# Optimization experiments

Hardware: AMD Instinct MI355X
Metric: run time of the kernel (lower is better)

The kernel has to match this reference:

```python
import jax, jax.numpy as jnp
import numpy as np
import math

N_HEAD = 16
N_EMBED = 1024
BLOCK_SIZE = 2048


def setup_inputs() -> dict:
    key = jax.random.key(0)
    k0, k1, k2, k3, k4 = jax.random.split(key, 5)
    B, T, C = 2, 2048, N_EMBED
    x = jax.random.normal(k0, (B, T, C), dtype=jnp.float32)
    # torch nn.Linear weights: [out_features, in_features]
    s_attn = 1.0 / math.sqrt(C)
    W_attn = jax.random.uniform(k1, (3 * C, C), dtype=jnp.float32, minval=-s_attn, maxval=s_attn)
    b_attn = jax.random.uniform(k2, (3 * C,), dtype=jnp.float32, minval=-s_attn, maxval=s_attn)
    W_proj = jax.random.uniform(k3, (C, C), dtype=jnp.float32, minval=-s_attn, maxval=s_attn)
    b_proj = jax.random.uniform(k4, (C,), dtype=jnp.float32, minval=-s_attn, maxval=s_attn)
    return {"x": x, "W_attn": W_attn, "b_attn": b_attn, "W_proj": W_proj, "b_proj": b_proj}


def reference(x, W_attn, b_attn, W_proj, b_proj):
    B, T, C = x.shape
    H = N_HEAD
    D = C // H
    qkv = x @ W_attn.T + b_attn                     # [B,T,3C]
    q, k, v = jnp.split(qkv, 3, axis=2)
    # [B,T,C] -> [B,H,T,D]
    q = q.reshape(B, T, H, D).transpose(0, 2, 1, 3)
    k = k.reshape(B, T, H, D).transpose(0, 2, 1, 3)
    v = v.reshape(B, T, H, D).transpose(0, 2, 1, 3)
    scale = 1.0 / math.sqrt(D)
    attn = jnp.einsum('bhqd,bhkd->bhqk', q, k) * scale   # [B,H,T,T]
    causal = jnp.tril(jnp.ones((T, T), dtype=bool))
    attn = jnp.where(causal[None, None, :, :], attn, -jnp.inf)
    attn = jax.nn.softmax(attn, axis=-1)
    y = jnp.einsum('bhqk,bhkd->bhqd', attn, v)           # [B,H,T,D]
    y = y.transpose(0, 2, 1, 3).reshape(B, T, C)
    return y @ W_proj.T + b_proj
```

## Files before the change

### kernel.cpp

```cpp
#include <hip/hip_runtime.h>
#include <hip/hip_bf16.h>

#define B_  2
#define T_  2048
#define C_  1024
#define H_  16
#define D_  64
#define M_  (B_*T_)
#define N1_ (3*C_)

typedef short bf16x8 __attribute__((ext_vector_type(8)));
typedef short bf16x4 __attribute__((ext_vector_type(4)));
typedef float f32x4 __attribute__((ext_vector_type(4)));
typedef unsigned short u16;
typedef u16 u16x8 __attribute__((ext_vector_type(8)));

#define QSCALE 0.18033688011112042f
#define C8     11.541560327111707f

__device__ __forceinline__ u16 f2bf(float f) {
  unsigned u = __float_as_uint(f);
  u += 0x7FFFu + ((u >> 16) & 1u);
  return (u16)(u >> 16);
}

__device__ __forceinline__ void gload16(const void* g, void* l) {
  __builtin_amdgcn_global_load_lds((__attribute__((address_space(1))) void*)g,
                                   (__attribute__((address_space(3))) void*)l,
                                   16, 0, 0);
}

__global__ __launch_bounds__(256) void cvt3(const float* __restrict__ x,
                                            const float* __restrict__ wa,
                                            const float* __restrict__ wp,
                                            u16* __restrict__ out) {
  int i = (blockIdx.x * 256 + threadIdx.x) * 8;
  const float* src;
  int off;
  if (i < M_ * C_)                 { src = x;  off = 0; }
  else if (i < M_ * C_ + N1_ * C_) { src = wa; off = M_ * C_; }
  else                             { src = wp; off = M_ * C_ + N1_ * C_; }
  float4 a = *(const float4*)(src + (i - off));
  float4 b = *(const float4*)(src + (i - off) + 4);
  u16x8 o;
  o[0] = f2bf(a.x); o[1] = f2bf(a.y); o[2] = f2bf(a.z); o[3] = f2bf(a.w);
  o[4] = f2bf(b.x); o[5] = f2bf(b.y); o[6] = f2bf(b.z); o[7] = f2bf(b.w);
  *(u16x8*)(out + i) = o;
}

__device__ __forceinline__ void gemm_core(const u16* __restrict__ A,
                                          const u16* __restrict__ W,
                                          u16* As, u16* Bs,
                                          f32x4 (&acc)[4][4],
                                          int m0, int n0, int K) {
  int tid = threadIdx.x;
  int lane = tid & 63, wid = tid >> 6;
  int wr = wid >> 1, wc = wid & 1;

  int arow = wid * 16 + (lane >> 2);
  int ag = lane & 3;
  int sg = ag ^ ((arow >> 1) & 3);
  const u16* aSrc0 = A + (m0 + arow) * K + sg * 8;
  const u16* aSrc1 = aSrc0 + 64 * K;
  const u16* bSrc0 = W + (n0 + arow) * K + sg * 8;
  const u16* bSrc1 = bSrc0 + 64 * K;
  u16* aDst0 = As + (wid * 16) * 32;
  u16* aDst1 = As + (64 + wid * 16) * 32;
  u16* bDst0 = Bs + (wid * 16) * 32;
  u16* bDst1 = Bs + (64 + wid * 16) * 32;

  int rg = lane >> 4;
  int aoff[4], boff[4];
#pragma unroll
  for (int m = 0; m < 4; ++m) {
    int row = wr * 64 + m * 16 + (lane & 15);
    aoff[m] = row * 32 + (rg ^ ((row >> 1) & 3)) * 8;
    row = wc * 64 + m * 16 + (lane & 15);
    boff[m] = row * 32 + (rg ^ ((row >> 1) & 3)) * 8;
  }

  for (int kt = 0; kt < K / 32; ++kt) {
    int k0 = kt * 32;
    __syncthreads();
    gload16(aSrc0 + k0, aDst0);
    gload16(aSrc1 + k0, aDst1);
    gload16(bSrc0 + k0, bDst0);
    gload16(bSrc1 + k0, bDst1);
    __syncthreads();

    bf16x8 af[4], bfr[4];
#pragma unroll
    for (int m = 0; m < 4; ++m) af[m] = *(const bf16x8*)(As + aoff[m]);
#pragma unroll
    for (int n = 0; n < 4; ++n) bfr[n] = *(const bf16x8*)(Bs + boff[n]);
#pragma unroll
    for (int m = 0; m < 4; ++m)
#pragma unroll
      for (int n = 0; n < 4; ++n)
        acc[m][n] = __builtin_amdgcn_mfma_f32_16x16x32_bf16(af[m], bfr[n], acc[m][n], 0, 0, 0);
  }
}

__global__ __launch_bounds__(256) void gemm_qkv(const u16* __restrict__ A,
                                                const u16* __restrict__ W,
                                                const float* __restrict__ bias,
                                                u16* __restrict__ Qb,
                                                u16* __restrict__ Kb,
                                                u16* __restrict__ Vt) {
  __shared__ __align__(16) u16 As[128 * 32];
  __shared__ __align__(16) u16 Bs[128 * 32];
  f32x4 acc[4][4] = {};
  int m0 = blockIdx.x * 128, n0 = blockIdx.y * 128;
  gemm_core(A, W, As, Bs, acc, m0, n0, C_);

  int lane = threadIdx.x & 63, wid = threadIdx.x >> 6;
  int wr = wid >> 1, wc = wid & 1;
  int rg = lane >> 4, cl = lane & 15;
#pragma unroll
  for (int n = 0; n < 4; ++n) {
    int gn = n0 + wc * 64 + n * 16 + cl;
    float bv = bias[gn];
    int seg = gn >> 10, cc = gn & 1023;
    int h = cc >> 6, d = cc & 63;
    float sc = (seg == 0) ? QSCALE : 1.0f;
#pragma unroll
    for (int m = 0; m < 4; ++m) {
#pragma unroll
      for (int r = 0; r < 4; ++r) {
        int gm = m0 + wr * 64 + m * 16 + rg * 4 + r;
        int b = gm >> 11, t = gm & 2047;
        u16 val = f2bf((acc[m][n][r] + bv) * sc);
        int bh = b * 16 + h;
        if (seg == 0)      Qb[(bh * 2048 + t) * 64 + d] = val;
        else if (seg == 1) Kb[(bh * 2048 + t) * 64 + d] = val;
        else               Vt[(bh * 64 + d) * 2048 + t] = val;
      }
    }
  }
}

__global__ __launch_bounds__(256) void gemm_proj(const u16* __restrict__ A,
                                                 const u16* __restrict__ W,
                                                 const float* __restrict__ bias,
                                                 float* __restrict__ out) {
  __shared__ __align__(16) u16 As[128 * 32];
  __shared__ __align__(16) u16 Bs[128 * 32];
  f32x4 acc[4][4] = {};
  int m0 = blockIdx.x * 128, n0 = blockIdx.y * 128;
  gemm_core(A, W, As, Bs, acc, m0, n0, C_);

  int lane = threadIdx.x & 63, wid = threadIdx.x >> 6;
  int wr = wid >> 1, wc = wid & 1;
  int rg = lane >> 4, cl = lane & 15;
#pragma unroll
  for (int n = 0; n < 4; ++n) {
    int gn = n0 + wc * 64 + n * 16 + cl;
    float bv = bias[gn];
#pragma unroll
    for (int m = 0; m < 4; ++m) {
#pragma unroll
      for (int r = 0; r < 4; ++r) {
        int gm = m0 + wr * 64 + m * 16 + rg * 4 + r;
        out[gm * 1024 + gn] = acc[m][n][r] + bv;
      }
    }
  }
}

__global__ __launch_bounds__(256, 2) void attn_fwd(const u16* __restrict__ Qb,
                                                   const u16* __restrict__ Kb,
                                                   const u16* __restrict__ Vt,
                                                   u16* __restrict__ Yb) {
  __shared__ __align__(16) u16 Ks[2][64 * 64];
  __shared__ __align__(16) u16 Vs[2][64 * 64];
  __shared__ __align__(16) u16 Ps[4][32 * 64];
  int tid = threadIdx.x, lane = tid & 63, w = tid >> 6;
  int cl = lane & 15, kg = lane >> 4;
  int bid = blockIdx.x;
  int bh = bid & 31;
  int i = bid >> 5;
  int qt = (i < 8) ? i : 23 - i;
  int qb0 = qt * 128 + w * 32;
  int jmaxw = (qb0 + 31) >> 6;
  int jmaxb = 2 * qt + 1;
  const u16* Qp = Qb + (size_t)bh * (2048 * 64);
  const u16* Kp = Kb + (size_t)bh * (2048 * 64);
  const u16* Vp = Vt + (size_t)bh * (64 * 2048);
  u16* Pw = Ps[w];

  int srow8 = lane >> 3;
  int sg = (lane & 7) ^ srow8;
  const u16* Ksrc = Kp + (w * 16 + srow8) * 64 + sg * 8;
  const u16* Vsrc = Vp + (w * 16 + srow8) * 2048 + sg * 8;

  bf16x8 qf[2][2];
#pragma unroll
  for (int fr = 0; fr < 2; ++fr)
#pragma unroll
    for (int dk = 0; dk < 2; ++dk)
      qf[fr][dk] = *(const bf16x8*)(Qp + (qb0 + fr * 16 + cl) * 64 + dk * 32 + kg * 8);

  f32x4 o[2][4] = {};
  float lsum[2] = {0.f, 0.f};
  const f32x4 CINIT = {-C8, -C8, -C8, -C8};

  auto STAGE = [&](int j, int buf) {
    u16* kd = &Ks[buf][w * 1024];
    u16* vd = &Vs[buf][w * 1024];
    const u16* ks = Ksrc + j * 4096;
    const u16* vs = Vsrc + j * 64;
    gload16(ks, kd);
    gload16(ks + 512, kd + 512);
    gload16(vs, vd);
    gload16(vs + 8 * 2048, vd + 512);
  };

  auto FULL = [&](int buf) {
    const u16* Kl = Ks[buf];
    const u16* Vl = Vs[buf];
    bf16x8 kf[4][2], vf[4][2];
#pragma unroll
    for (int fc = 0; fc < 4; ++fc) {
      int row = fc * 16 + cl;
      kf[fc][0] = *(const bf16x8*)(Kl + row * 64 + (((0 * 4 + kg) ^ (cl & 7)) * 8));
      kf[fc][1] = *(const bf16x8*)(Kl + row * 64 + (((1 * 4 + kg) ^ (cl & 7)) * 8));
    }
#pragma unroll
    for (int dc = 0; dc < 4; ++dc) {
      int row = dc * 16 + cl;
      vf[dc][0] = *(const bf16x8*)(Vl + row * 64 + (((0 * 4 + kg) ^ (cl & 7)) * 8));
      vf[dc][1] = *(const bf16x8*)(Vl + row * 64 + (((1 * 4 + kg) ^ (cl & 7)) * 8));
    }
    f32x4 s[2][4];
#pragma unroll
    for (int fc = 0; fc < 4; ++fc)
#pragma unroll
      for (int fr = 0; fr < 2; ++fr) {
        f32x4 z = CINIT;
        z = __builtin_amdgcn_mfma_f32_16x16x32_bf16(kf[fc][0], qf[fr][0], z, 0, 0, 0);
        z = __builtin_amdgcn_mfma_f32_16x16x32_bf16(kf[fc][1], qf[fr][1], z, 0, 0, 0);
        s[fr][fc] = z;
      }
#pragma unroll
    for (int fr = 0; fr < 2; ++fr) {
      int rowb = (fr * 16 + cl) * 64;
#pragma unroll
      for (int fc = 0; fc < 4; ++fc) {
        float p0 = exp2f(s[fr][fc][0]);
        float p1 = exp2f(s[fr][fc][1]);
        float p2 = exp2f(s[fr][fc][2]);
        float p3 = exp2f(s[fr][fc][3]);
        lsum[fr] += (p0 + p1) + (p2 + p3);
        union { bf16x4 v; __hip_bfloat162 h[2]; } pk;
        pk.h[0] = __float22bfloat162_rn(make_float2(p0, p1));
        pk.h[1] = __float22bfloat162_rn(make_float2(p2, p3));
        *(bf16x4*)(Pw + rowb + (((fc * 2 + (kg >> 1)) ^ (cl & 7)) * 8) + (kg & 1) * 4) = pk.v;
      }
    }
    bf16x8 pf[2][2];
#pragma unroll
    for (int fr = 0; fr < 2; ++fr) {
      int rowb = (fr * 16 + cl) * 64;
      pf[fr][0] = *(const bf16x8*)(Pw + rowb + ((kg ^ (cl & 7)) * 8));
      pf[fr][1] = *(const bf16x8*)(Pw + rowb + (((kg + 4) ^ (cl & 7)) * 8));
    }
#pragma unroll
    for (int kv2 = 0; kv2 < 2; ++kv2)
#pragma unroll
      for (int dc = 0; dc < 4; ++dc) {
        o[0][dc] = __builtin_amdgcn_mfma_f32_16x16x32_bf16(pf[0][kv2], vf[dc][kv2], o[0][dc], 0, 0, 0);
        o[1][dc] = __builtin_amdgcn_mfma_f32_16x16x32_bf16(pf[1][kv2], vf[dc][kv2], o[1][dc], 0, 0, 0);
      }
  };

  auto EDGE = [&](int buf, int j) {
    const u16* Kl = Ks[buf];
    const u16* Vl = Vs[buf];
    int par = w & 1;
    int fcTop = par ? 3 : 1;
    int kvTop = par;
    bf16x8 kf[4][2], vf[4][2];
#pragma unroll
    for (int fc = 0; fc < 4; ++fc)
      if (fc <= fcTop) {
        int row = fc * 16 + cl;
        kf[fc][0] = *(const bf16x8*)(Kl + row * 64 + ((kg ^ (cl & 7)) * 8));
        kf[fc][1] = *(const bf16x8*)(Kl + row * 64 + (((4 + kg) ^ (cl & 7)) * 8));
      }
#pragma unroll
    for (int dc = 0; dc < 4; ++dc) {
      int row = dc * 16 + cl;
      vf[dc][0] = *(const bf16x8*)(Vl + row * 64 + ((kg ^ (cl & 7)) * 8));
      if (kvTop) vf[dc][1] = *(const bf16x8*)(Vl + row * 64 + (((4 + kg) ^ (cl & 7)) * 8));
    }
    f32x4 s[2][4];
#pragma unroll
    for (int fc = 0; fc < 4; ++fc)
      if (fc <= fcTop) {
#pragma unroll
        for (int fr = 0; fr < 2; ++fr) {
          f32x4 z = CINIT;
          z = __builtin_amdgcn_mfma_f32_16x16x32_bf16(kf[fc][0], qf[fr][0], z, 0, 0, 0);
          z = __builtin_amdgcn_mfma_f32_16x16x32_bf16(kf[fc][1], qf[fr][1], z, 0, 0, 0);
          s[fr][fc] = z;
        }
      }
#pragma unroll
    for (int fr = 0; fr < 2; ++fr) {
      int rowb = (fr * 16 + cl) * 64;
      int qg = qb0 + fr * 16 + cl;
#pragma unroll
      for (int fc = 0; fc < 4; ++fc) {
        bf16x4 pw;
        if (fc <= fcTop) {
#pragma unroll
          for (int r = 0; r < 4; ++r) {
            int kvg = j * 64 + fc * 16 + kg * 4 + r;
            float p = (kvg <= qg) ? exp2f(s[fr][fc][r]) : 0.f;
            lsum[fr] += p;
            pw[r] = (short)f2bf(p);
          }
        } else {
          pw[0] = 0; pw[1] = 0; pw[2] = 0; pw[3] = 0;
        }
        *(bf16x4*)(Pw + rowb + (((fc * 2 + (kg >> 1)) ^ (cl & 7)) * 8) + (kg & 1) * 4) = pw;
      }
    }
    bf16x8 pf[2][2];
#pragma unroll
    for (int fr = 0; fr < 2; ++fr) {
      int rowb = (fr * 16 + cl) * 64;
      pf[fr][0] = *(const bf16x8*)(Pw + rowb + ((kg ^ (cl & 7)) * 8));
      if (kvTop) pf[fr][1] = *(const bf16x8*)(Pw + rowb + (((kg + 4) ^ (cl & 7)) * 8));
    }
#pragma unroll
    for (int kv2 = 0; kv2 < 2; ++kv2)
      if (kv2 <= kvTop) {
#pragma unroll
        for (int dc = 0; dc < 4; ++dc) {
          o[0][dc] = __builtin_amdgcn_mfma_f32_16x16x32_bf16(pf[0][kv2], vf[dc][kv2], o[0][dc], 0, 0, 0);
          o[1][dc] = __builtin_amdgcn_mfma_f32_16x16x32_bf16(pf[1][kv2], vf[dc][kv2], o[1][dc], 0, 0, 0);
        }
      }
  };

  STAGE(0, 0);
  __syncthreads();
  int buf = 0;
  for (int j = 0; j <= jmaxb; ++j) {
    if (j < jmaxb) STAGE(j + 1, buf ^ 1);
    if (j < jmaxw)       FULL(buf);
    else if (j == jmaxw) EDGE(buf, j);
    __syncthreads();
    buf ^= 1;
  }

  int b = bh >> 4, h = bh & 15;
#pragma unroll
  for (int fr = 0; fr < 2; ++fr) {
    float l = lsum[fr];
    l += __shfl_xor(l, 16);
    l += __shfl_xor(l, 32);
    float linv = 1.f / l;
    float li[4];
#pragma unroll
    for (int r = 0; r < 4; ++r) li[r] = __shfl(linv, kg * 4 + r);
#pragma unroll
    for (int dc = 0; dc < 4; ++dc)
#pragma unroll
      for (int r = 0; r < 4; ++r) {
        int t = qb0 + fr * 16 + kg * 4 + r;
        int d = dc * 16 + cl;
        Yb[((size_t)(b * 2048 + t)) * 1024 + h * 64 + d] = f2bf(o[fr][dc][r] * li[r]);
      }
  }
}

extern "C" void kernel_launch(void* const* d_in, const int* in_sizes, int n_in,
                              void* d_out, int out_size, void* d_ws, size_t ws_size,
                              hipStream_t stream) {
  const float* x  = (const float*)d_in[0];
  const float* Wa = (const float*)d_in[1];
  const float* ba = (const float*)d_in[2];
  const float* Wp = (const float*)d_in[3];
  const float* bp = (const float*)d_in[4];
  float* out = (float*)d_out;

  u16* xb  = (u16*)d_ws;
  u16* Wab = xb  + (size_t)M_ * C_;
  u16* Wpb = Wab + (size_t)N1_ * C_;
  u16* Qb  = Wpb + (size_t)C_ * C_;
  u16* Kb  = Qb  + (size_t)M_ * C_;
  u16* Vt  = Kb  + (size_t)M_ * C_;
  u16* Yb  = Vt  + (size_t)M_ * C_;

  cvt3<<<(M_ * C_ + N1_ * C_ + C_ * C_) / 2048, 256, 0, stream>>>(x, Wa, Wp, xb);
  gemm_qkv<<<dim3(M_ / 128, N1_ / 128), 256, 0, stream>>>(xb, Wab, ba, Qb, Kb, Vt);
  attn_fwd<<<512, 256, 0, stream>>>(Qb, Kb, Vt, Yb);
  gemm_proj<<<dim3(M_ / 128, C_ / 128), 256, 0, stream>>>(Yb, Wpb, bp, out);
}
```

Baseline: 116.6 us.

## Widen GEMM K-tile to 64 and stage V transpose through LDS for coalesced stores

The shared GEMM core now loads 128x64 K-tiles instead of 128x32, halving the number of barrier-separated load/compute iterations and issuing two MFMA k-steps per tile with an 8-way XOR swizzle. In the QKV GEMM, blocks producing V now write the biased tile into LDS transposed, then emit 16-byte vector stores along the time axis into Vt, replacing scattered 2-byte strided stores. LDS use per GEMM block doubles to 32 KB, which may limit occupancy. The attention-kernel index edits are cosmetic.

Measured after the change: 123.7 us. 1.06x slower.

```diff
diff --git a/kernel.cpp b/kernel.cpp
--- a/kernel.cpp
+++ b/kernel.cpp
@@ -57,47 +57,48 @@
   int lane = tid & 63, wid = tid >> 6;
   int wr = wid >> 1, wc = wid & 1;
 
-  int arow = wid * 16 + (lane >> 2);
-  int ag = lane & 3;
-  int sg = ag ^ ((arow >> 1) & 3);
-  const u16* aSrc0 = A + (m0 + arow) * K + sg * 8;
-  const u16* aSrc1 = aSrc0 + 64 * K;
-  const u16* bSrc0 = W + (n0 + arow) * K + sg * 8;
-  const u16* bSrc1 = bSrc0 + 64 * K;
-  u16* aDst0 = As + (wid * 16) * 32;
-  u16* aDst1 = As + (64 + wid * 16) * 32;
-  u16* bDst0 = Bs + (wid * 16) * 32;
-  u16* bDst1 = Bs + (64 + wid * 16) * 32;
-
-  int rg = lane >> 4;
-  int aoff[4], boff[4];
+  int srow = lane >> 3;
+  int sg = (lane & 7) ^ srow;
+  const u16* aSrc = A + (size_t)(m0 + wid * 32 + srow) * K + sg * 8;
+  const u16* bSrc = W + (size_t)(n0 + wid * 32 + srow) * K + sg * 8;
+  u16* aDst = As + (wid * 32) * 64;
+  u16* bDst = Bs + (wid * 32) * 64;
+
+  int rg = lane >> 4, cl = lane & 15;
+  int arb[4], ar7[4], brb[4], br7[4];
 #pragma unroll
   for (int m = 0; m < 4; ++m) {
-    int row = wr * 64 + m * 16 + (lane & 15);
-    aoff[m] = row * 32 + (rg ^ ((row >> 1) & 3)) * 8;
-    row = wc * 64 + m * 16 + (lane & 15);
-    boff[m] = row * 32 + (rg ^ ((row >> 1) & 3)) * 8;
-  }
-
-  for (int kt = 0; kt < K / 32; ++kt) {
-    int k0 = kt * 32;
+    int row = wr * 64 + m * 16 + cl;
+    arb[m] = row * 64; ar7[m] = row & 7;
+    row = wc * 64 + m * 16 + cl;
+    brb[m] = row * 64; br7[m] = row & 7;
+  }
+
+  for (int kt = 0; kt < K / 64; ++kt) {
+    int k0 = kt * 64;
     __syncthreads();
-    gload16(aSrc0 + k0, aDst0);
-    gload16(aSrc1 + k0, aDst1);
-    gload16(bSrc0 + k0, bDst0);
-    gload16(bSrc1 + k0, bDst1);
+#pragma unroll
+    for (int i = 0; i < 4; ++i) {
+      gload16(aSrc + (size_t)i * 8 * K + k0, aDst + i * 8 * 64);
+      gload16(bSrc + (size_t)i * 8 * K + k0, bDst + i * 8 * 64);
+    }
     __syncthreads();
 
-    bf16x8 af[4], bfr[4];
-#pragma unroll
-    for (int m = 0; m < 4; ++m) af[m] = *(const bf16x8*)(As + aoff[m]);
-#pragma unroll
-    for (int n = 0; n < 4; ++n) bfr[n] = *(const bf16x8*)(Bs + boff[n]);
-#pragma unroll
-    for (int m = 0; m < 4; ++m)
+#pragma unroll
+    for (int kh = 0; kh < 2; ++kh) {
+      bf16x8 af[4], bfr[4];
+#pragma unroll
+      for (int m = 0; m < 4; ++m)
+        af[m] = *(const bf16x8*)(As + arb[m] + (((kh * 4 + rg) ^ ar7[m]) * 8));
 #pragma unroll
       for (int n = 0; n < 4; ++n)
-        acc[m][n] = __builtin_amdgcn_mfma_f32_16x16x32_bf16(af[m], bfr[n], acc[m][n], 0, 0, 0);
+        bfr[n] = *(const bf16x8*)(Bs + brb[n] + (((kh * 4 + rg) ^ br7[n]) * 8));
+#pragma unroll
+      for (int m = 0; m < 4; ++m)
+#pragma unroll
+        for (int n = 0; n < 4; ++n)
+          acc[m][n] = __builtin_amdgcn_mfma_f32_16x16x32_bf16(af[m], bfr[n], acc[m][n], 0, 0, 0);
+    }
   }
 }
 
@@ -107,34 +108,62 @@
                                                 u16* __restrict__ Qb,
                                                 u16* __restrict__ Kb,
                                                 u16* __restrict__ Vt) {
-  __shared__ __align__(16) u16 As[128 * 32];
-  __shared__ __align__(16) u16 Bs[128 * 32];
+  __shared__ __align__(16) u16 Sh[2][128 * 64];
   f32x4 acc[4][4] = {};
   int m0 = blockIdx.x * 128, n0 = blockIdx.y * 128;
-  gemm_core(A, W, As, Bs, acc, m0, n0, C_);
-
-  int lane = threadIdx.x & 63, wid = threadIdx.x >> 6;
+  gemm_core(A, W, Sh[0], Sh[1], acc, m0, n0, C_);
+
+  int tid = threadIdx.x;
+  int lane = tid & 63, wid = tid >> 6;
   int wr = wid >> 1, wc = wid & 1;
   int rg = lane >> 4, cl = lane & 15;
-#pragma unroll
-  for (int n = 0; n < 4; ++n) {
-    int gn = n0 + wc * 64 + n * 16 + cl;
-    float bv = bias[gn];
-    int seg = gn >> 10, cc = gn & 1023;
-    int h = cc >> 6, d = cc & 63;
+  int seg = n0 >> 10;
+
+  if (seg < 2) {
     float sc = (seg == 0) ? QSCALE : 1.0f;
 #pragma unroll
-    for (int m = 0; m < 4; ++m) {
-#pragma unroll
-      for (int r = 0; r < 4; ++r) {
-        int gm = m0 + wr * 64 + m * 16 + rg * 4 + r;
-        int b = gm >> 11, t = gm & 2047;
-        u16 val = f2bf((acc[m][n][r] + bv) * sc);
-        int bh = b * 16 + h;
-        if (seg == 0)      Qb[(bh * 2048 + t) * 64 + d] = val;
-        else if (seg == 1) Kb[(bh * 2048 + t) * 64 + d] = val;
-        else               Vt[(bh * 64 + d) * 2048 + t] = val;
-      }
+    for (int n = 0; n < 4; ++n) {
+      int gn = n0 + wc * 64 + n * 16 + cl;
+      float bv = bias[gn];
+      int cc = gn & 1023;
+      int h = cc >> 6, d = cc & 63;
+#pragma unroll
+      for (int m = 0; m < 4; ++m) {
+#pragma unroll
+        for (int r = 0; r < 4; ++r) {
+          int gm = m0 + wr * 64 + m * 16 + rg * 4 + r;
+          int b = gm >> 11, t = gm & 2047;
+          u16 val = f2bf((acc[m][n][r] + bv) * sc);
+          int bh = b * 16 + h;
+          if (seg == 0) Qb[((size_t)(bh * 2048 + t)) * 64 + d] = val;
+          else          Kb[((size_t)(bh * 2048 + t)) * 64 + d] = val;
+        }
+      }
+    }
+  } else {
+    __syncthreads();
+    u16* Tr = &Sh[0][0];
+#pragma unroll
+    for (int n = 0; n < 4; ++n) {
+      int gnl = wc * 64 + n * 16 + cl;
+      float bv = bias[n0 + gnl];
+#pragma unroll
+      for (int m = 0; m < 4; ++m)
+#pragma unroll
+        for (int r = 0; r < 4; ++r)
+          Tr[gnl * 128 + wr * 64 + m * 16 + rg * 4 + r] = f2bf(acc[m][n][r] + bv);
+    }
+    __syncthreads();
+    int b = m0 >> 11, t0 = m0 & 2047;
+    int ccb = n0 - 2048;
+#pragma unroll
+    for (int it = 0; it < 8; ++it) {
+      int idx = it * 256 + tid;
+      int dl = idx >> 4, oct = idx & 15;
+      int cc = ccb + dl;
+      int bh = b * 16 + (cc >> 6), d = cc & 63;
+      *(u16x8*)(Vt + ((size_t)(bh * 64 + d)) * 2048 + t0 + oct * 8) =
+          *(const u16x8*)(Tr + dl * 128 + oct * 8);
     }
   }
 }
@@ -143,11 +172,10 @@
                                                  const u16* __restrict__ W,
                                                  const float* __restrict__ bias,
                                                  float* __restrict__ out) {
-  __shared__ __align__(16) u16 As[128 * 32];
-  __shared__ __align__(16) u16 Bs[128 * 32];
+  __shared__ __align__(16) u16 Sh[2][128 * 64];
   f32x4 acc[4][4] = {};
   int m0 = blockIdx.x * 128, n0 = blockIdx.y * 128;
-  gemm_core(A, W, As, Bs, acc, m0, n0, C_);
+  gemm_core(A, W, Sh[0], Sh[1], acc, m0, n0, C_);
 
   int lane = threadIdx.x & 63, wid = threadIdx.x >> 6;
   int wr = wid >> 1, wc = wid & 1;
@@ -161,7 +189,7 @@
 #pragma unroll
       for (int r = 0; r < 4; ++r) {
         int gm = m0 + wr * 64 + m * 16 + rg * 4 + r;
-        out[gm * 1024 + gn] = acc[m][n][r] + bv;
+        out[(size_t)gm * 1024 + gn] = acc[m][n][r] + bv;
       }
     }
   }
@@ -222,14 +250,14 @@
 #pragma unroll
     for (int fc = 0; fc < 4; ++fc) {
       int row = fc * 16 + cl;
-      kf[fc][0] = *(const bf16x8*)(Kl + row * 64 + (((0 * 4 + kg) ^ (cl & 7)) * 8));
-      kf[fc][1] = *(const bf16x8*)(Kl + row * 64 + (((1 * 4 + kg) ^ (cl & 7)) * 8));
+      kf[fc][0] = *(const bf16x8*)(Kl + row * 64 + ((kg ^ (cl & 7)) * 8));
+      kf[fc][1] = *(const bf16x8*)(Kl + row * 64 + (((4 + kg) ^ (cl & 7)) * 8));
     }
 #pragma unroll
     for (int dc = 0; dc < 4; ++dc) {
       int row = dc * 16 + cl;
-      vf[dc][0] = *(const bf16x8*)(Vl + row * 64 + (((0 * 4 + kg) ^ (cl & 7)) * 8));
-      vf[dc][1] = *(const bf16x8*)(Vl + row * 64 + (((1 * 4 + kg) ^ (cl & 7)) * 8));
+      vf[dc][0] = *(const bf16x8*)(Vl + row * 64 + ((kg ^ (cl & 7)) * 8));
+      vf[dc][1] = *(const bf16x8*)(Vl + row * 64 + (((4 + kg) ^ (cl & 7)) * 8));
     }
     f32x4 s[2][4];
 #pragma unroll
```
